# Performance work log

Hardware: AMD Instinct MI355X
Metric: run time of the kernel (lower is better)

The kernel has to match this reference:

```python
import jax, jax.numpy as jnp
import numpy as np

I, H, O, T = 1024, 1024, 512, 8192


def setup_inputs() -> dict:
    key = jax.random.key(0)
    ks = jax.random.split(key, 7)
    s_ih = 1.0 / np.sqrt(H)
    return {
        "x": jax.random.normal(ks[0], (T, 1, I), dtype=jnp.float32),
        "W_ih": jax.random.uniform(ks[1], (4 * H, I), jnp.float32, -s_ih, s_ih),
        "W_hh": jax.random.uniform(ks[2], (4 * H, H), jnp.float32, -s_ih, s_ih),
        "b_ih": jax.random.uniform(ks[3], (4 * H,), jnp.float32, -s_ih, s_ih),
        "b_hh": jax.random.uniform(ks[4], (4 * H,), jnp.float32, -s_ih, s_ih),
        "W_out": jax.random.uniform(ks[5], (O, H), jnp.float32, -s_ih, s_ih),
        "b_out": jax.random.uniform(ks[6], (O,), jnp.float32, -s_ih, s_ih),
    }


def reference(x, W_ih, W_hh, b_ih, b_hh, W_out, b_out):
    # x: [T, 1, I] -> [T, I] (batch=1)
    xs = x.reshape(x.shape[0], -1)
    Hs = W_hh.shape[1]
    # Precompute input contribution to gates for all timesteps: [T, 4H]
    px = xs @ W_ih.T + b_ih + b_hh

    def step(carry, px_t):
        h, c = carry
        gates = px_t + h @ W_hh.T  # [4H]
        i = jax.nn.sigmoid(gates[0 * Hs:1 * Hs])
        f = jax.nn.sigmoid(gates[1 * Hs:2 * Hs])
        g = jnp.tanh(gates[2 * Hs:3 * Hs])
        o = jax.nn.sigmoid(gates[3 * Hs:4 * Hs])
        c_new = f * c + i * g
        h_new = o * jnp.tanh(c_new)
        return (h_new, c_new), h_new

    h0 = jnp.zeros((Hs,), dtype=x.dtype)
    c0 = jnp.zeros((Hs,), dtype=x.dtype)
    _, lstm_out = jax.lax.scan(step, (h0, c0), px)  # [T, H]

    logits = lstm_out @ W_out.T + b_out  # [T, O]
    # Original applies LogSoftmax over dim=0 (the sequence dim)
    return jax.nn.log_softmax(logits, axis=0)
```

## Files before the change

kernel.cpp:

```cpp
#include <hip/hip_runtime.h>
#include <stdint.h>

#define NT   8192
#define HID  1024
#define NWG  128

typedef _Float16 f16x2 __attribute__((ext_vector_type(2)));
__device__ __forceinline__ uint32_t f16_bits(float a) {
    return (uint32_t)__builtin_bit_cast(uint16_t, (_Float16)a);
}
__device__ __forceinline__ float f16_lo(uint32_t w) {
    return (float)__builtin_bit_cast(_Float16, (uint16_t)(w & 0xffffu));
}
__device__ __forceinline__ float f16_hi(uint32_t w) {
    return (float)__builtin_bit_cast(_Float16, (uint16_t)(w >> 16));
}
__device__ __forceinline__ uint32_t pack_f16(float a, float b) {
    return f16_bits(a) | (f16_bits(b) << 16);
}
__device__ __forceinline__ float dot2(uint32_t a, uint32_t b, float c) {
    return __builtin_amdgcn_fdot2(__builtin_bit_cast(f16x2, a),
                                  __builtin_bit_cast(f16x2, b), c, false);
}
__device__ __forceinline__ float fast_rcp(float x) { return __builtin_amdgcn_rcpf(x); }
__device__ __forceinline__ float fast_sig(float x) { return fast_rcp(1.f + __expf(-x)); }
__device__ __forceinline__ float fast_tanh(float x) {
    return 1.f - 2.f * fast_rcp(1.f + __expf(2.f * x));
}

__global__ void prep_bias(const float* __restrict__ a, const float* __restrict__ b,
                          float* __restrict__ o) {
    int i = blockIdx.x * 256 + threadIdx.x;
    if (i < 4096) o[i] = a[i] + b[i];
}

__global__ void prep_whh(const float* __restrict__ Whh, uint32_t* __restrict__ wpk) {
    int idx = blockIdx.x * 256 + threadIdx.x;
    int u    = idx & 511;
    int lr   = (idx >> 9) & 31;
    int w    = idx >> 14;
    int v    = lr >> 3;
    int gate = (lr >> 1) & 3;
    int jj   = lr & 1;
    int R = gate * 1024 + w * 8 + 2 * v + jj;
    const float* rp = Whh + (size_t)R * 1024 + 2 * u;
    wpk[idx] = pack_f16(rp[0], rp[1]);
}

template <bool PACK_OUT>
__launch_bounds__(256)
__global__ void gemm_bt(const float* __restrict__ A, const float* __restrict__ B,
                        const float* __restrict__ bias, void* __restrict__ outp,
                        int N, int K) {
    __shared__ float As[16 * 132];
    __shared__ float Bs[16 * 132];
    const int tid = threadIdx.x;
    const int bm = blockIdx.x, bn = blockIdx.y;
    const int tx = tid & 15, ty = tid >> 4;
    const int r = tid >> 2, cf = tid & 3;

    float acc[8][8];
#pragma unroll
    for (int i = 0; i < 8; ++i)
#pragma unroll
        for (int j = 0; j < 8; ++j) acc[i][j] = 0.f;

    const float* Ap = A + (size_t)(bm * 128 + r) * K + cf * 4;
    const float* Bp = B + (size_t)(bn * 128 + r) * K + cf * 4;

    for (int k0 = 0; k0 < K; k0 += 16) {
        float4 a0 = *(const float4*)(Ap + k0);
        float4 a1 = *(const float4*)(Ap + (size_t)64 * K + k0);
        float4 b0 = *(const float4*)(Bp + k0);
        float4 b1 = *(const float4*)(Bp + (size_t)64 * K + k0);
        __syncthreads();
#pragma unroll
        for (int e = 0; e < 4; ++e) {
            As[(cf * 4 + e) * 132 + r]      = ((const float*)&a0)[e];
            As[(cf * 4 + e) * 132 + r + 64] = ((const float*)&a1)[e];
            Bs[(cf * 4 + e) * 132 + r]      = ((const float*)&b0)[e];
            Bs[(cf * 4 + e) * 132 + r + 64] = ((const float*)&b1)[e];
        }
        __syncthreads();
#pragma unroll
        for (int k = 0; k < 16; ++k) {
            const float4 av0 = *(const float4*)&As[k * 132 + ty * 8];
            const float4 av1 = *(const float4*)&As[k * 132 + ty * 8 + 4];
            const float4 bv0 = *(const float4*)&Bs[k * 132 + tx * 4];
            const float4 bv1 = *(const float4*)&Bs[k * 132 + tx * 4 + 64];
            const float a[8] = {av0.x, av0.y, av0.z, av0.w, av1.x, av1.y, av1.z, av1.w};
            const float b[8] = {bv0.x, bv0.y, bv0.z, bv0.w, bv1.x, bv1.y, bv1.z, bv1.w};
#pragma unroll
            for (int i = 0; i < 8; ++i)
#pragma unroll
                for (int j = 0; j < 8; ++j) acc[i][j] = fmaf(a[i], b[j], acc[i][j]);
        }
    }

    const int mb = bm * 128 + ty * 8;
    const int n0 = bn * 128 + tx * 4, n1 = n0 + 64;
    float bb[8];
#pragma unroll
    for (int j = 0; j < 4; ++j) { bb[j] = bias[n0 + j]; bb[4 + j] = bias[n1 + j]; }

    if (PACK_OUT) {
        uint32_t* o = (uint32_t*)outp;
        const int halfN = N >> 1;
#pragma unroll
        for (int i = 0; i < 8; ++i) {
            uint2 w0, w1;
            w0.x = pack_f16(acc[i][0] + bb[0], acc[i][1] + bb[1]);
            w0.y = pack_f16(acc[i][2] + bb[2], acc[i][3] + bb[3]);
            w1.x = pack_f16(acc[i][4] + bb[4], acc[i][5] + bb[5]);
            w1.y = pack_f16(acc[i][6] + bb[6], acc[i][7] + bb[7]);
            *(uint2*)(o + (size_t)(mb + i) * halfN + (n0 >> 1)) = w0;
            *(uint2*)(o + (size_t)(mb + i) * halfN + (n1 >> 1)) = w1;
        }
    } else {
        float* o = (float*)outp;
#pragma unroll
        for (int i = 0; i < 8; ++i) {
            float4 v0, v1;
            v0.x = acc[i][0] + bb[0]; v0.y = acc[i][1] + bb[1];
            v0.z = acc[i][2] + bb[2]; v0.w = acc[i][3] + bb[3];
            v1.x = acc[i][4] + bb[4]; v1.y = acc[i][5] + bb[5];
            v1.z = acc[i][6] + bb[6]; v1.w = acc[i][7] + bb[7];
            *(float4*)(o + (size_t)(mb + i) * N + n0) = v0;
            *(float4*)(o + (size_t)(mb + i) * N + n1) = v1;
        }
    }
}

__launch_bounds__(256)
__global__ void lstm_rec(const uint32_t* __restrict__ wpk, const uint32_t* __restrict__ pxp,
                         uint32_t* htag, float* __restrict__ lstm_out) {
    const int tid = threadIdx.x, w = blockIdx.x;
    const int wave = tid >> 6, L = tid & 63;

    uint32_t wreg[8][8];
    {
        const uint32_t* wb = wpk + (size_t)w * 16384 + (size_t)(wave * 8) * 512 + L;
#pragma unroll
        for (int rr = 0; rr < 8; ++rr)
#pragma unroll
            for (int m = 0; m < 8; ++m)
                wreg[rr][m] = wb[rr * 512 + m * 64];
    }

    float c0 = 0.f;
    uint64_t* buf0 = (uint64_t*)htag;
    uint64_t* buf1 = (uint64_t*)(htag + 1024);

    for (int t = 0; t < NT; ++t) {
        const uint32_t tg = (uint32_t)t;
        uint64_t* srcb = (t & 1) ? buf1 : buf0;
        uint32_t* dstb = (uint32_t*)((t & 1) ? buf0 : buf1);
        const uint64_t tagpat = ((uint64_t)tg << 16) | ((uint64_t)tg << 48);

        float pxv[4] = {0.f, 0.f, 0.f, 0.f};
        if (L < 2) {
#pragma unroll
            for (int g = 0; g < 4; ++g) {
                int R = g * 1024 + w * 8 + 2 * wave + L;
                uint32_t pw = pxp[(size_t)t * 2048 + (R >> 1)];
                pxv[g] = (R & 1) ? f16_hi(pw) : f16_lo(pw);
            }
        }

        uint64_t hp[8];
        bool mydone = false;
        int tries = 0;
        for (;;) {
            if (!mydone) {
#pragma unroll
                for (int m = 0; m < 8; ++m)
                    hp[m] = __hip_atomic_load(srcb + (L + 64 * m),
                                              __ATOMIC_RELAXED, __HIP_MEMORY_SCOPE_AGENT);
                int ok = 1;
#pragma unroll
                for (int m = 0; m < 8; ++m)
                    ok &= ((hp[m] & 0xffff0000ffff0000ull) == tagpat);
                mydone = (ok != 0);
            }
            if (__all(mydone)) break;
            if (++tries > (1 << 15)) break;
        }

        uint32_t hk[8];
#pragma unroll
        for (int m = 0; m < 8; ++m)
            hk[m] = ((uint32_t)hp[m] & 0xffffu) | (((uint32_t)(hp[m] >> 32)) << 16);

        float acc[8];
#pragma unroll
        for (int rr = 0; rr < 8; ++rr) {
            float a = 0.f;
#pragma unroll
            for (int m = 0; m < 8; ++m) a = dot2(wreg[rr][m], hk[m], a);
            acc[rr] = a;
        }

#pragma unroll
        for (int bit = 4; bit >= 1; bit >>= 1) {
#pragma unroll
            for (int i = 0; i < bit; ++i) {
                float v0 = acc[i], v1 = acc[i + bit];
                float send = (L & bit) ? v0 : v1;
                float recv = __shfl_xor(send, bit, 64);
                acc[i] = ((L & bit) ? v1 : v0) + recv;
            }
        }
        float tot = acc[0];
        tot += __shfl_xor(tot, 8, 64);
        tot += __shfl_xor(tot, 16, 64);
        tot += __shfl_xor(tot, 32, 64);
        float r0 = __shfl(tot, (L & 1), 64);
        float r1 = __shfl(tot, (L & 1) + 2, 64);
        float r2 = __shfl(tot, (L & 1) + 4, 64);
        float r3 = __shfl(tot, (L & 1) + 6, 64);

        if (L < 2) {
            float gi = r0 + pxv[0];
            float gf = r1 + pxv[1];
            float gg = r2 + pxv[2];
            float go = r3 + pxv[3];
            float iv = fast_sig(gi);
            float fv = fast_sig(gf);
            float gv = fast_tanh(gg);
            float ov = fast_sig(go);
            c0 = fv * c0 + iv * gv;
            float h = ov * fast_tanh(c0);
            int j = w * 8 + 2 * wave + L;
            uint32_t word = f16_bits(h) | ((uint32_t)(t + 1) << 16);
            __hip_atomic_store(dstb + j, word, __ATOMIC_RELAXED, __HIP_MEMORY_SCOPE_AGENT);
            lstm_out[(size_t)t * 1024 + j] = h;
        }
    }
}

__global__ void sm_partial(const float* __restrict__ logits, float* __restrict__ pM,
                           float* __restrict__ pS) {
    const int cb = blockIdx.x, rb = blockIdx.y, tid = threadIdx.x;
    const int c = cb * 64 + (tid & 63);
    const int r0 = rb * 256 + (tid >> 6) * 64;
    const float* p = logits + (size_t)r0 * 512 + c;
    float m = -1e30f;
    for (int k = 0; k < 64; ++k) m = fmaxf(m, p[(size_t)k * 512]);
    float s = 0.f;
    for (int k = 0; k < 64; ++k) s += __expf(p[(size_t)k * 512] - m);
    __shared__ float sM[4][64], sS[4][64];
    sM[tid >> 6][tid & 63] = m;
    sS[tid >> 6][tid & 63] = s;
    __syncthreads();
    if (tid < 64) {
        float M = sM[0][tid];
        for (int i = 1; i < 4; ++i) M = fmaxf(M, sM[i][tid]);
        float S = 0.f;
        for (int i = 0; i < 4; ++i) S += sS[i][tid] * __expf(sM[i][tid] - M);
        pM[rb * 512 + cb * 64 + tid] = M;
        pS[rb * 512 + cb * 64 + tid] = S;
    }
}

__global__ void sm_combine(const float* __restrict__ pM, const float* __restrict__ pS,
                           float* __restrict__ cc) {
    const int c = threadIdx.x;
    float M = -1e30f;
    for (int i = 0; i < 32; ++i) M = fmaxf(M, pM[i * 512 + c]);
    float S = 0.f;
    for (int i = 0; i < 32; ++i) S += pS[i * 512 + c] * __expf(pM[i * 512 + c] - M);
    cc[c] = M + logf(S);
}

__global__ void sm_apply(float* __restrict__ out, const float* __restrict__ cc) {
    const int idx = blockIdx.x * 256 + threadIdx.x;
    float4 v = ((const float4*)out)[idx];
    float4 b = ((const float4*)cc)[idx & 127];
    v.x -= b.x; v.y -= b.y; v.z -= b.z; v.w -= b.w;
    ((float4*)out)[idx] = v;
}

extern "C" void kernel_launch(void* const* d_in, const int* in_sizes, int n_in,
                              void* d_out, int out_size, void* d_ws, size_t ws_size,
                              hipStream_t stream) {
    (void)in_sizes; (void)n_in; (void)out_size; (void)ws_size;
    const float* x    = (const float*)d_in[0];
    const float* Wih  = (const float*)d_in[1];
    const float* Whh  = (const float*)d_in[2];
    const float* bih  = (const float*)d_in[3];
    const float* bhh  = (const float*)d_in[4];
    const float* Wout = (const float*)d_in[5];
    const float* bout = (const float*)d_in[6];
    float* out = (float*)d_out;

    char* ws = (char*)d_ws;
    uint32_t* pxp   = (uint32_t*)(ws + 0ull);
    uint32_t* wpk   = (uint32_t*)(ws + 67108864ull);
    float* lstm_out = (float*)   (ws + 75497472ull);
    float* biasc    = (float*)   (ws + 109051904ull);
    uint32_t* htag  = (uint32_t*)(ws + 109068288ull);
    float* pM       = (float*)   (ws + 109076480ull);
    float* pS       = (float*)   (ws + 109142016ull);
    float* cc       = (float*)   (ws + 109207552ull);

    hipMemsetAsync(htag, 0, 8192, stream);

    prep_whh<<<8192, 256, 0, stream>>>(Whh, wpk);
    prep_bias<<<16, 256, 0, stream>>>(bih, bhh, biasc);

    gemm_bt<true><<<dim3(64, 32), 256, 0, stream>>>(x, Wih, biasc, (void*)pxp, 4096, 1024);

    lstm_rec<<<NWG, 256, 0, stream>>>(wpk, pxp, htag, lstm_out);

    gemm_bt<false><<<dim3(64, 4), 256, 0, stream>>>(lstm_out, Wout, bout, (void*)out, 512, 1024);

    sm_partial<<<dim3(8, 32), 256, 0, stream>>>(out, pM, pS);
    sm_combine<<<1, 512, 0, stream>>>(pM, pS, cc);
    sm_apply<<<4096, 256, 0, stream>>>(out, cc);
}
```

Baseline: 16.46 ms.

## Split h-vector polling across waves and share via LDS

```diff
diff --git a/kernel.cpp b/kernel.cpp
--- a/kernel.cpp
+++ b/kernel.cpp
@@ -134,6 +134,7 @@
 __launch_bounds__(256)
 __global__ void lstm_rec(const uint32_t* __restrict__ wpk, const uint32_t* __restrict__ pxp,
                          uint32_t* htag, float* __restrict__ lstm_out) {
+    __shared__ uint32_t Hl[2][512];
     const int tid = threadIdx.x, w = blockIdx.x;
     const int wave = tid >> 6, L = tid & 63;
 
@@ -148,12 +149,14 @@
     }
 
     float c0 = 0.f;
-    uint64_t* buf0 = (uint64_t*)htag;
-    uint64_t* buf1 = (uint64_t*)(htag + 1024);
+    const uint64_t* buf0 = (const uint64_t*)htag;
+    const uint64_t* buf1 = buf0 + 512;
+    const int q0 = 128 * wave + 2 * L;
+    int tw = 0;
 
     for (int t = 0; t < NT; ++t) {
         const uint32_t tg = (uint32_t)t;
-        uint64_t* srcb = (t & 1) ? buf1 : buf0;
+        const uint64_t* srcb = (t & 1) ? buf1 : buf0;
         uint32_t* dstb = (uint32_t*)((t & 1) ? buf0 : buf1);
         const uint64_t tagpat = ((uint64_t)tg << 16) | ((uint64_t)tg << 48);
 
@@ -167,29 +170,31 @@
             }
         }
 
-        uint64_t hp[8];
-        bool mydone = false;
+        uint64_t ha = 0, hb = 0;
+        bool done = false;
         int tries = 0;
         for (;;) {
-            if (!mydone) {
-#pragma unroll
-                for (int m = 0; m < 8; ++m)
-                    hp[m] = __hip_atomic_load(srcb + (L + 64 * m),
-                                              __ATOMIC_RELAXED, __HIP_MEMORY_SCOPE_AGENT);
-                int ok = 1;
-#pragma unroll
-                for (int m = 0; m < 8; ++m)
-                    ok &= ((hp[m] & 0xffff0000ffff0000ull) == tagpat);
-                mydone = (ok != 0);
+            if (!done) {
+                ha = __hip_atomic_load(srcb + q0,     __ATOMIC_RELAXED,
+                                       __HIP_MEMORY_SCOPE_AGENT);
+                hb = __hip_atomic_load(srcb + q0 + 1, __ATOMIC_RELAXED,
+                                       __HIP_MEMORY_SCOPE_AGENT);
+                done = ((ha & 0xffff0000ffff0000ull) == tagpat) &
+                       ((hb & 0xffff0000ffff0000ull) == tagpat);
             }
-            if (__all(mydone)) break;
-            if (++tries > (1 << 15)) break;
-        }
+            if (__all(done)) break;
+            if (++tries > (1 << 13) || tw + tries > (1 << 17)) break;
+        }
+        tw += tries;
+
+        uint32_t* Hb = Hl[t & 1];
+        Hb[q0]     = ((uint32_t)ha & 0xffffu) | (((uint32_t)(ha >> 32)) << 16);
+        Hb[q0 + 1] = ((uint32_t)hb & 0xffffu) | (((uint32_t)(hb >> 32)) << 16);
+        __syncthreads();
 
         uint32_t hk[8];
 #pragma unroll
-        for (int m = 0; m < 8; ++m)
-            hk[m] = ((uint32_t)hp[m] & 0xffffu) | (((uint32_t)(hp[m] >> 32)) << 16);
+        for (int m = 0; m < 8; ++m) hk[m] = Hb[L + 64 * m];
 
         float acc[8];
 #pragma unroll
```

After: 14.76 ms. 10.4% less time.
